# Kernel optimization log

Hardware: AMD Instinct MI355X
Metric: run time of the kernel (lower is better)

The kernel has to match this reference:

```python
import jax, jax.numpy as jnp
import numpy as np

B = 16
C = 80
LEVELS = [(128, 128, 8), (64, 64, 16), (32, 32, 32), (16, 16, 64), (8, 8, 128)]
TOPN = 1000
MIN_SCORE = 0.05
NMS_THR = 0.6
MAX_OBJ = 100


def setup_inputs() -> dict:
    key = jax.random.key(0)
    inp = {}
    for l, (H, W, s) in enumerate(LEVELS):
        key, k1, k2, k3 = jax.random.split(key, 4)
        inp[f"cls{l}"] = jax.random.uniform(k1, (B, H, W, C), jnp.float32)
        inp[f"reg{l}"] = jax.random.uniform(k2, (B, H, W, 4), jnp.float32) * 128.0
        inp[f"ctr{l}"] = jax.random.uniform(k3, (B, H, W, 1), jnp.float32)
        xs = (jnp.arange(W, dtype=jnp.float32) + 0.5) * s
        ys = (jnp.arange(H, dtype=jnp.float32) + 0.5) * s
        gx, gy = jnp.meshgrid(xs, ys)  # [H, W]
        pos = jnp.stack([gx, gy], axis=-1)  # [H, W, 2]
        inp[f"pos{l}"] = jnp.broadcast_to(pos, (B, H, W, 2))
    return inp


def _nms_one(scores, classes, bboxes):
    # scores [N], classes int32 [N], bboxes float [N, 4] (already int-truncated values)
    s = jnp.where(scores > MIN_SCORE, scores, -jnp.inf)  # score-threshold mask
    top_s, top_i = jax.lax.top_k(s, TOPN)  # sort descending, keep topn
    top_c = jax.lax.stop_gradient(classes[top_i].astype(jnp.float32))
    top_b = bboxes[top_i]
    valid = top_s > MIN_SCORE
    wh = top_b[:, 2:4] - top_b[:, 0:2]
    areas = jnp.clip(wh[:, 0] * wh[:, 1], 0.0001)
    ar = jnp.arange(TOPN)

    def body(i, suppressed):
        active = valid[i] & (~suppressed[i])
        b = top_b[i]
        tl = jnp.maximum(b[0:2], top_b[:, 0:2])
        br = jnp.minimum(b[2:4], top_b[:, 2:4])
        owh = jnp.clip(br - tl, 0.0)
        inter = owh[:, 0] * owh[:, 1]
        union = jnp.clip(areas[i] + areas - inter, 0.0001)
        iou = inter / union
        return suppressed | (active & (ar > i) & (iou >= NMS_THR))

    suppressed = jax.lax.fori_loop(0, TOPN, body, jnp.zeros((TOPN,), bool))
    keep = valid & (~suppressed)
    rank = jnp.cumsum(keep.astype(jnp.int32)) - 1
    # scatter kept detections (in score order) into first MAX_OBJ slots; slot MAX_OBJ is a dump
    idx = jnp.where(keep & (rank < MAX_OBJ), rank, MAX_OBJ)
    out_s = jnp.full((MAX_OBJ + 1,), -1.0, jnp.float32).at[idx].set(jnp.where(keep, top_s, -1.0))[:MAX_OBJ]
    out_c = jnp.full((MAX_OBJ + 1,), -1.0, jnp.float32).at[idx].set(jnp.where(keep, top_c, -1.0))[:MAX_OBJ]
    out_b = jnp.zeros((MAX_OBJ + 1, 4), jnp.float32).at[idx].set(jnp.where(keep[:, None], top_b, 0.0))[:MAX_OBJ]
    return out_s, out_c, out_b


def _forward(cls_list, reg_list, ctr_list, pos_list):
    ss, cc, bb = [], [], []
    for c, r, t, p in zip(cls_list, reg_list, ctr_list, pos_list):
        b = c.shape[0]
        c = c.reshape(b, -1, c.shape[-1])   # [B, HW, 80]
        r = r.reshape(b, -1, 4)             # [B, HW, 4]
        t = t.reshape(b, -1)                # [B, HW]
        p = p.reshape(b, -1, 2)             # [B, HW, 2]
        sc = jnp.sqrt(jnp.max(c, axis=2) * t)
        cl = jnp.argmax(c, axis=2).astype(jnp.int32)
        bmin = p - r[:, :, 0:2]
        bmax = p + r[:, :, 2:4]
        # torch .int() truncates toward zero; values are used as floats afterward
        box = jax.lax.stop_gradient(jnp.trunc(jnp.concatenate([bmin, bmax], axis=2)))
        ss.append(sc); cc.append(cl); bb.append(box)
    scores = jnp.concatenate(ss, axis=1)
    classes = jnp.concatenate(cc, axis=1)
    boxes = jnp.concatenate(bb, axis=1)
    return jax.vmap(_nms_one)(scores, classes, boxes)


def reference(cls0, cls1, cls2, cls3, cls4, reg0, reg1, reg2, reg3, reg4,
              ctr0, ctr1, ctr2, ctr3, ctr4, pos0, pos1, pos2, pos3, pos4):
    return _forward([cls0, cls1, cls2, cls3, cls4],
                    [reg0, reg1, reg2, reg3, reg4],
                    [ctr0, ctr1, ctr2, ctr3, ctr4],
                    [pos0, pos1, pos2, pos3, pos4])
```

## Files before the change

kernel.cpp:

```cpp
#include <hip/hip_runtime.h>
#include <stdint.h>

typedef unsigned int u32;
typedef unsigned long long u64;

#define NTOT 21824
#define NBATCH 16
#define TOPN 1000
#define MAXOBJ 100
#define CAPC 8192
#define NBINS 32768

__global__ __launch_bounds__(1024) void zero_kernel(u32* __restrict__ h) {
    int i = blockIdx.x * 1024 + threadIdx.x;
    if (i < NBATCH * NBINS + NBATCH * 32) h[i] = 0;
}

__global__ __launch_bounds__(256) void decode_kernel(
    const float* __restrict__ cls0, const float* __restrict__ cls1,
    const float* __restrict__ cls2, const float* __restrict__ cls3,
    const float* __restrict__ cls4,
    const float* __restrict__ ctr0, const float* __restrict__ ctr1,
    const float* __restrict__ ctr2, const float* __restrict__ ctr3,
    const float* __restrict__ ctr4,
    u32* __restrict__ keys, int* __restrict__ clsidx, u32* __restrict__ hist)
{
    int tid = threadIdx.x;
    int g = tid >> 2, j = tid & 3;
    int loc = blockIdx.x * 64 + g;
    int b = blockIdx.y;
    if (loc >= NTOT) return;

    const float *cp, *tp;
    if (loc < 16384)      { size_t o = (size_t)b*16384 + loc;          cp = cls0 + o*80; tp = ctr0 + o; }
    else if (loc < 20480) { size_t o = (size_t)b*4096  + (loc-16384);  cp = cls1 + o*80; tp = ctr1 + o; }
    else if (loc < 21504) { size_t o = (size_t)b*1024  + (loc-20480);  cp = cls2 + o*80; tp = ctr2 + o; }
    else if (loc < 21760) { size_t o = (size_t)b*256   + (loc-21504);  cp = cls3 + o*80; tp = ctr3 + o; }
    else                  { size_t o = (size_t)b*64    + (loc-21760);  cp = cls4 + o*80; tp = ctr4 + o; }

    const float4* c4 = (const float4*)cp;
    float maxv = -1.0f; int arg = 0;
#pragma unroll
    for (int q = 0; q < 5; ++q) {
        float4 v = c4[j + 4*q];
        int ch = 16*q + 4*j;
        if (v.x > maxv) { maxv = v.x; arg = ch;     }
        if (v.y > maxv) { maxv = v.y; arg = ch + 1; }
        if (v.z > maxv) { maxv = v.z; arg = ch + 2; }
        if (v.w > maxv) { maxv = v.w; arg = ch + 3; }
    }
#pragma unroll
    for (int d = 1; d <= 2; d <<= 1) {
        float ov = __shfl_xor(maxv, d);
        int   oa = __shfl_xor(arg, d);
        if (ov > maxv || (ov == maxv && oa < arg)) { maxv = ov; arg = oa; }
    }
    if (j == 0) {
        float score = sqrtf(maxv * (*tp));
        u32 key = (score > 0.05f) ? (__float_as_uint(score) | 0x80000000u) : 0u;
        size_t o = (size_t)b * NTOT + loc;
        keys[o] = key;
        clsidx[o] = arg;
        if (key) atomicAdd(&hist[b * NBINS + ((key >> 16) & (NBINS - 1))], 1u);
    }
}

__global__ __launch_bounds__(1024) void pivot_kernel(
    const u32* __restrict__ hist, u32* __restrict__ params,
    float* __restrict__ tscore, float* __restrict__ tcls, float4* __restrict__ tbox)
{
    __shared__ u32 s_wtot[16];
    __shared__ int s_tf;
    int b = blockIdx.x, tid = threadIdx.x;
    int lane = tid & 63, wave = tid >> 6;
    const u32* hb = hist + (size_t)b * NBINS;
    int base = tid * 32;

    for (int i = tid; i < TOPN; i += 1024) {
        size_t o = (size_t)b * TOPN + i;
        tscore[o] = -1.0f; tcls[o] = -1.0f;
        tbox[o] = make_float4(0.f, 0.f, 0.f, 0.f);
    }
    if (tid == 0) s_tf = -1;

    u32 s = 0;
#pragma unroll 8
    for (int j = 0; j < 32; ++j) s += hb[base + j];

    u32 x = s;
#pragma unroll
    for (int off = 1; off < 64; off <<= 1) {
        u32 y = __shfl_down(x, off);
        if (lane + off < 64) x += y;
    }
    if (lane == 0) s_wtot[wave] = x;
    __syncthreads();
    u32 wsuf = 0, tot = 0;
    for (int w2 = 0; w2 < 16; ++w2) { u32 v = s_wtot[w2]; tot += v; if (w2 > wave) wsuf += v; }
    u32 suffix_incl = x + wsuf;
    u32 suffix_above = suffix_incl - s;
    u32 target = (tot < TOPN) ? tot : TOPN;

    if (target > 0 && suffix_incl >= target) {
        u32 run = suffix_above;
        for (int j = 31; j >= 0; --j) {
            run += hb[base + j];
            if (run >= target) { atomicMax(&s_tf, base + j); break; }
        }
    }
    __syncthreads();
    if (tid == 0) {
        int t0 = s_tf;
        u32 P;
        if (target == 0)        P = 0xFFFFFFFFu;
        else if (tot <= TOPN)   P = 1u;
        else                    P = ((u32)t0 << 16) | 0x80000000u;
        params[2 * b] = P;
        params[2 * b + 1] = target;
    }
}

__global__ __launch_bounds__(256) void gather_kernel(
    const u32* __restrict__ keys, const u32* __restrict__ params,
    u64* __restrict__ candbuf, u32* __restrict__ gcnt)
{
    __shared__ u32 s_wcnt[4];
    __shared__ u32 s_base;
    int b = blockIdx.y;
    int tid = threadIdx.x;
    int lane = tid & 63, wave = tid >> 6;
    u32 P = params[2 * b];
    int i = blockIdx.x * 256 + tid;
    u32 k = (i < NTOT) ? keys[(size_t)b * NTOT + i] : 0u;
    bool pass = (k != 0u) && (k >= P);
    u64 mask = __ballot(pass);
    if (lane == 0) s_wcnt[wave] = (u32)__popcll(mask);
    __syncthreads();
    if (tid == 0) {
        u32 tot = s_wcnt[0] + s_wcnt[1] + s_wcnt[2] + s_wcnt[3];
        s_base = tot ? atomicAdd(&gcnt[b * 32], tot) : 0u;
    }
    __syncthreads();
    if (pass) {
        u32 woff = 0;
        for (int w2 = 0; w2 < wave; ++w2) woff += s_wcnt[w2];
        u32 pos = s_base + woff + (u32)__popcll(mask & ((1ull << lane) - 1ull));
        if (pos < CAPC)
            candbuf[(size_t)b * CAPC + pos] = ((u64)k << 32) | (u32)(~i);
    }
}

__global__ __launch_bounds__(256) void rank_kernel(
    const u64* __restrict__ candbuf, const u32* __restrict__ gcnt,
    const u32* __restrict__ params,
    const int* __restrict__ clsidx,
    const float* __restrict__ reg0, const float* __restrict__ reg1,
    const float* __restrict__ reg2, const float* __restrict__ reg3,
    const float* __restrict__ reg4,
    float* __restrict__ tscore, float* __restrict__ tcls, float4* __restrict__ tbox)
{
    int b = blockIdx.y;
    int lane = threadIdx.x & 63;
    u32 M = gcnt[b * 32]; if (M > CAPC) M = CAPC;
    u32 target = params[2 * b + 1];
    const u64* cb = candbuf + (size_t)b * CAPC;
    u32 Mr = (M + 63u) & ~63u;

    u32 wbase0 = blockIdx.x * 256 + (threadIdx.x & ~63u);
    for (u32 base = wbase0; base < M; base += 8 * 256) {
        u32 i0 = base + lane;
        bool val = (i0 < M);
        u64 e = val ? cb[i0] : ~0ull;
        u32 r = 0;
        for (u32 c0 = 0; c0 < Mr; c0 += 64) {
            u32 j = c0 + lane;
            u64 v = (j < M) ? cb[j] : 0ull;
            u32 vlo = (u32)v, vhi = (u32)(v >> 32);
#pragma unroll
            for (int s = 0; s < 64; ++s) {
                u32 lo = (u32)__builtin_amdgcn_readlane((int)vlo, s);
                u32 hi = (u32)__builtin_amdgcn_readlane((int)vhi, s);
                u64 vj = ((u64)hi << 32) | lo;
                r += (vj > e) ? 1u : 0u;
            }
        }
        if (val && r < target) {
            u32 k = (u32)(e >> 32);
            u32 loc = ~(u32)e;
            const float* rp; float st; u32 li; int wsh;
            if (loc < 16384u)      { li = loc;          wsh = 7; st = 8.f;   rp = reg0 + ((size_t)b*16384 + li)*4; }
            else if (loc < 20480u) { li = loc - 16384u; wsh = 6; st = 16.f;  rp = reg1 + ((size_t)b*4096  + li)*4; }
            else if (loc < 21504u) { li = loc - 20480u; wsh = 5; st = 32.f;  rp = reg2 + ((size_t)b*1024  + li)*4; }
            else if (loc < 21760u) { li = loc - 21504u; wsh = 4; st = 64.f;  rp = reg3 + ((size_t)b*256   + li)*4; }
            else                   { li = loc - 21760u; wsh = 3; st = 128.f; rp = reg4 + ((size_t)b*64    + li)*4; }
            u32 wx = li & ((1u << wsh) - 1u);
            u32 hy = li >> wsh;
            float px = ((float)wx + 0.5f) * st;
            float py = ((float)hy + 0.5f) * st;
            float4 rg = *(const float4*)rp;
            float4 bx;
            bx.x = truncf(px - rg.x); bx.y = truncf(py - rg.y);
            bx.z = truncf(px + rg.z); bx.w = truncf(py + rg.w);
            size_t src = (size_t)b * NTOT + loc;
            size_t o = (size_t)b * TOPN + r;
            tscore[o] = __uint_as_float(k & 0x7FFFFFFFu);
            tcls[o] = (float)clsidx[src];
            tbox[o] = bx;
        }
    }
}

__global__ __launch_bounds__(256) void iou_kernel(
    const float4* __restrict__ tbox, u64* __restrict__ sup)
{
    __shared__ float4 sbox[TOPN];
    int b = blockIdx.y;
    int tid = threadIdx.x, lane = tid & 63, wave = tid >> 6;
    const float4* tb = tbox + (size_t)b * TOPN;
    for (int i = tid; i < TOPN; i += 256) sbox[i] = tb[i];
    __syncthreads();
    int i = blockIdx.x * 4 + wave;
    float4 bi = sbox[i];
    float areai = fmaxf((bi.z - bi.x) * (bi.w - bi.y), 0.0001f);
    u64* row = sup + ((size_t)b * TOPN + i) * 16;
#pragma unroll
    for (int w = 0; w < 16; ++w) {
        int col = w * 64 + lane;
        bool bit = false;
        if (col < TOPN) {
            float4 bj = sbox[col];
            float areaj = fmaxf((bj.z - bj.x) * (bj.w - bj.y), 0.0001f);
            float tlx = fmaxf(bi.x, bj.x), tly = fmaxf(bi.y, bj.y);
            float brx = fminf(bi.z, bj.z), bry = fminf(bi.w, bj.w);
            float ow = fmaxf(brx - tlx, 0.f), oh = fmaxf(bry - tly, 0.f);
            float inter = ow * oh;
            float uni = fmaxf(areai + areaj - inter, 0.0001f);
            bit = (col > i) && (inter / uni >= 0.6f);
        }
        u64 m = __ballot(bit);
        if (lane == 0) row[w] = m;
    }
}

#define CHROWS 128
#define NCHUNK 8

__global__ __launch_bounds__(1024) void finalize_kernel(
    const float* __restrict__ tscore, const float* __restrict__ tcls,
    const float4* __restrict__ tbox, const u64* __restrict__ sup,
    float* __restrict__ out)
{
    __shared__ u64 mat[2][CHROWS * 16];
    __shared__ u32 validsh[TOPN];
    __shared__ u64 removed_sh[16];
    __shared__ u32 wpref[17];
    int b = blockIdx.x, tid = threadIdx.x;
    int wave = tid >> 6, lane = tid & 63;

    for (int i = tid; i < TOPN; i += 1024)
        validsh[i] = (tscore[(size_t)b * TOPN + i] > 0.05f) ? 1u : 0u;

    const u64* supb = sup + (size_t)b * TOPN * 16;
    for (int idx = tid; idx < CHROWS * 16; idx += 1024)
        mat[0][idx] = supb[idx];
    __syncthreads();

    u64 my = 0;
    if (wave == 0) {
#pragma unroll
        for (int w2 = 0; w2 < 16; ++w2) {
            int i = w2 * 64 + lane;
            bool v = (i < TOPN) ? (validsh[i] != 0) : false;
            u64 m = __ballot(v);
            if (lane == w2) my = ~m;
        }
    }

    for (int chunk = 0; chunk < NCHUNK; ++chunk) {
        if (wave > 0 && chunk + 1 < NCHUNK) {
            int nr = (chunk + 1 == NCHUNK - 1) ? (TOPN - (NCHUNK - 1) * CHROWS) : CHROWS;
            const u64* src = supb + (size_t)(chunk + 1) * CHROWS * 16;
            u64* dst = mat[(chunk + 1) & 1];
            for (int idx = tid - 64; idx < nr * 16; idx += 960)
                dst[idx] = src[idx];
        }
        if (wave == 0) {
            int r0 = chunk * CHROWS;
            int rows = (chunk == NCHUNK - 1) ? (TOPN - r0) : CHROWS;
            int lw = lane & 15;
            const u64* M = mat[chunk & 1];
            for (int sub = 0; sub < rows; sub += 64) {
                int w2 = (r0 + sub) >> 6;
                u64 cur = __shfl(my, w2);
                int nsub = rows - sub; if (nsub > 64) nsub = 64;
                const u64* R = M + sub * 16;
                int ngrp = nsub >> 3;
                u64 cme[8], cww[8];
#pragma unroll
                for (int g = 0; g < 8; ++g) { cme[g] = R[g*16 + lw]; cww[g] = R[g*16 + w2]; }
                for (int grp = 0; grp < ngrp; ++grp) {
                    u64 nme[8] = {0,0,0,0,0,0,0,0}, nww[8] = {0,0,0,0,0,0,0,0};
                    if (grp + 1 < ngrp) {
                        const u64* Rn = R + (grp + 1) * 128;
#pragma unroll
                        for (int g = 0; g < 8; ++g) { nme[g] = Rn[g*16 + lw]; nww[g] = Rn[g*16 + w2]; }
                    }
#pragma unroll
                    for (int g = 0; g < 8; ++g) {
                        int u = grp * 8 + g;
                        u64 bit = (cur >> u) & 1ull;
                        u64 act = bit - 1ull;
                        cur |= cww[g] & act;
                        my  |= cme[g] & act;
                    }
#pragma unroll
                    for (int g = 0; g < 8; ++g) { cme[g] = nme[g]; cww[g] = nww[g]; }
                }
            }
        }
        __syncthreads();
    }
    if (wave == 0) {
        if (lane < 16) removed_sh[lane] = my;
        u32 pc = (lane < 16) ? (u32)__popcll(~my) : 0u;
#pragma unroll
        for (int off = 1; off < 16; off <<= 1) {
            u32 y = __shfl_up(pc, off);
            if (lane >= off) pc += y;
        }
        if (lane < 16) wpref[lane + 1] = pc;
        if (lane == 0) wpref[0] = 0;
    }
    __syncthreads();

    float* out_s = out;
    float* out_c = out + NBATCH * MAXOBJ;
    float* out_b = out + 2 * NBATCH * MAXOBJ;
    if (tid < MAXOBJ)     { out_s[b * MAXOBJ + tid] = -1.f; out_c[b * MAXOBJ + tid] = -1.f; }
    if (tid < MAXOBJ * 4) out_b[b * MAXOBJ * 4 + tid] = 0.f;
    __syncthreads();
    if (tid < TOPN) {
        u64 kw = ~removed_sh[tid >> 6];
        if ((kw >> (tid & 63)) & 1ull) {
            int rank = (int)wpref[tid >> 6] + (int)__popcll(kw & ((1ull << (tid & 63)) - 1ull));
            if (rank < MAXOBJ) {
                size_t o = (size_t)b * TOPN + tid;
                out_s[b * MAXOBJ + rank] = tscore[o];
                out_c[b * MAXOBJ + rank] = tcls[o];
                ((float4*)out_b)[b * MAXOBJ + rank] = tbox[o];
            }
        }
    }
}

extern "C" void kernel_launch(void* const* d_in, const int* in_sizes, int n_in,
                              void* d_out, int out_size, void* d_ws, size_t ws_size,
                              hipStream_t stream) {
    (void)in_sizes; (void)n_in; (void)out_size; (void)ws_size;
    const float* cls[5]; const float* reg[5]; const float* ctr[5];
    for (int l = 0; l < 5; ++l) {
        cls[l] = (const float*)d_in[4 * l + 0];
        reg[l] = (const float*)d_in[4 * l + 1];
        ctr[l] = (const float*)d_in[4 * l + 2];
    }
    char* w = (char*)d_ws;
    u32*    keys   = (u32*)(w + 0);
    int*    clsidx = (int*)(w + 1396736);
    float*  tscore = (float*)(w + 2793472);
    float*  tcls   = (float*)(w + 2857472);
    float4* tbox   = (float4*)(w + 2921472);
    u64*    sup    = (u64*)(w + 3177472);
    u64*    candbuf= (u64*)(w + 3177472);
    u32*    hist   = (u32*)(w + 5225472);
    u32*    gcnt   = (u32*)(w + 7322624);
    u32*    params = (u32*)(w + 7324672);

    zero_kernel<<<(NBATCH * NBINS + NBATCH * 32 + 1023) / 1024, 1024, 0, stream>>>(hist);
    decode_kernel<<<dim3((NTOT + 63) / 64, NBATCH), 256, 0, stream>>>(
        cls[0], cls[1], cls[2], cls[3], cls[4],
        ctr[0], ctr[1], ctr[2], ctr[3], ctr[4],
        keys, clsidx, hist);
    pivot_kernel<<<NBATCH, 1024, 0, stream>>>(hist, params, tscore, tcls, tbox);
    gather_kernel<<<dim3((NTOT + 255) / 256, NBATCH), 256, 0, stream>>>(keys, params, candbuf, gcnt);
    rank_kernel<<<dim3(8, NBATCH), 256, 0, stream>>>(candbuf, gcnt, params, clsidx,
                                                     reg[0], reg[1], reg[2], reg[3], reg[4],
                                                     tscore, tcls, tbox);
    iou_kernel<<<dim3(TOPN / 4, NBATCH), 256, 0, stream>>>(tbox, sup);
    finalize_kernel<<<NBATCH, 1024, 0, stream>>>(tscore, tcls, tbox, sup, (float*)d_out);
}
```

Before: 295.9 us.

## Move score histogram into pivot kernel shared memory and drop zero kernel

Removes the global 32768-bin histogram and its zeroing kernel. The pivot kernel now reads the keys and builds a 1024-bin histogram in shared memory over a clamped exponent range starting at BINBASE. The decode kernel has no atomics and processes two locations per thread group so more loads are in flight. The cost is that each pivot block scans all keys for its batch serially, and clamping to the lowest bin assumes scores sit within the binned range, which the score threshold and sqrt keep true.

```diff
diff --git a/kernel.cpp b/kernel.cpp
--- a/kernel.cpp
+++ b/kernel.cpp
@@ -9,11 +9,24 @@
 #define TOPN 1000
 #define MAXOBJ 100
 #define CAPC 8192
-#define NBINS 32768
-
-__global__ __launch_bounds__(1024) void zero_kernel(u32* __restrict__ h) {
-    int i = blockIdx.x * 1024 + threadIdx.x;
-    if (i < NBATCH * NBINS + NBATCH * 32) h[i] = 0;
+#define BINBASE 15616
+#define NBINS 1024
+
+__device__ __forceinline__ void locate(
+    int b, int loc,
+    const float* __restrict__ cls0, const float* __restrict__ cls1,
+    const float* __restrict__ cls2, const float* __restrict__ cls3,
+    const float* __restrict__ cls4,
+    const float* __restrict__ ctr0, const float* __restrict__ ctr1,
+    const float* __restrict__ ctr2, const float* __restrict__ ctr3,
+    const float* __restrict__ ctr4,
+    const float*& cp, const float*& tp)
+{
+    if (loc < 16384)      { size_t o = (size_t)b*16384 + loc;          cp = cls0 + o*80; tp = ctr0 + o; }
+    else if (loc < 20480) { size_t o = (size_t)b*4096  + (loc-16384);  cp = cls1 + o*80; tp = ctr1 + o; }
+    else if (loc < 21504) { size_t o = (size_t)b*1024  + (loc-20480);  cp = cls2 + o*80; tp = ctr2 + o; }
+    else if (loc < 21760) { size_t o = (size_t)b*256   + (loc-21504);  cp = cls3 + o*80; tp = ctr3 + o; }
+    else                  { size_t o = (size_t)b*64    + (loc-21760);  cp = cls4 + o*80; tp = ctr4 + o; }
 }
 
 __global__ __launch_bounds__(256) void decode_kernel(
@@ -23,71 +36,106 @@
     const float* __restrict__ ctr0, const float* __restrict__ ctr1,
     const float* __restrict__ ctr2, const float* __restrict__ ctr3,
     const float* __restrict__ ctr4,
-    u32* __restrict__ keys, int* __restrict__ clsidx, u32* __restrict__ hist)
+    u32* __restrict__ keys, int* __restrict__ clsidx)
 {
     int tid = threadIdx.x;
     int g = tid >> 2, j = tid & 3;
-    int loc = blockIdx.x * 64 + g;
     int b = blockIdx.y;
-    if (loc >= NTOT) return;
-
-    const float *cp, *tp;
-    if (loc < 16384)      { size_t o = (size_t)b*16384 + loc;          cp = cls0 + o*80; tp = ctr0 + o; }
-    else if (loc < 20480) { size_t o = (size_t)b*4096  + (loc-16384);  cp = cls1 + o*80; tp = ctr1 + o; }
-    else if (loc < 21504) { size_t o = (size_t)b*1024  + (loc-20480);  cp = cls2 + o*80; tp = ctr2 + o; }
-    else if (loc < 21760) { size_t o = (size_t)b*256   + (loc-21504);  cp = cls3 + o*80; tp = ctr3 + o; }
-    else                  { size_t o = (size_t)b*64    + (loc-21760);  cp = cls4 + o*80; tp = ctr4 + o; }
-
-    const float4* c4 = (const float4*)cp;
-    float maxv = -1.0f; int arg = 0;
+    int loc0 = blockIdx.x * 128 + g;
+    int loc1 = loc0 + 64;
+    bool v1 = (loc1 < NTOT);
+
+    const float *cp0, *tp0, *cp1, *tp1;
+    locate(b, loc0, cls0, cls1, cls2, cls3, cls4, ctr0, ctr1, ctr2, ctr3, ctr4, cp0, tp0);
+    locate(b, v1 ? loc1 : loc0, cls0, cls1, cls2, cls3, cls4, ctr0, ctr1, ctr2, ctr3, ctr4, cp1, tp1);
+
+    const float4* c40 = (const float4*)cp0;
+    const float4* c41 = (const float4*)cp1;
+    float4 a0[5], a1[5];
+#pragma unroll
+    for (int q = 0; q < 5; ++q) a0[q] = c40[j + 4*q];
+#pragma unroll
+    for (int q = 0; q < 5; ++q) a1[q] = c41[j + 4*q];
+    float t0v = *tp0;
+    float t1v = *tp1;
+
+    float maxv0 = -1.0f; int arg0 = 0;
+    float maxv1 = -1.0f; int arg1 = 0;
 #pragma unroll
     for (int q = 0; q < 5; ++q) {
-        float4 v = c4[j + 4*q];
+        float4 v = a0[q];
         int ch = 16*q + 4*j;
-        if (v.x > maxv) { maxv = v.x; arg = ch;     }
-        if (v.y > maxv) { maxv = v.y; arg = ch + 1; }
-        if (v.z > maxv) { maxv = v.z; arg = ch + 2; }
-        if (v.w > maxv) { maxv = v.w; arg = ch + 3; }
+        if (v.x > maxv0) { maxv0 = v.x; arg0 = ch;     }
+        if (v.y > maxv0) { maxv0 = v.y; arg0 = ch + 1; }
+        if (v.z > maxv0) { maxv0 = v.z; arg0 = ch + 2; }
+        if (v.w > maxv0) { maxv0 = v.w; arg0 = ch + 3; }
+    }
+#pragma unroll
+    for (int q = 0; q < 5; ++q) {
+        float4 v = a1[q];
+        int ch = 16*q + 4*j;
+        if (v.x > maxv1) { maxv1 = v.x; arg1 = ch;     }
+        if (v.y > maxv1) { maxv1 = v.y; arg1 = ch + 1; }
+        if (v.z > maxv1) { maxv1 = v.z; arg1 = ch + 2; }
+        if (v.w > maxv1) { maxv1 = v.w; arg1 = ch + 3; }
     }
 #pragma unroll
     for (int d = 1; d <= 2; d <<= 1) {
-        float ov = __shfl_xor(maxv, d);
-        int   oa = __shfl_xor(arg, d);
-        if (ov > maxv || (ov == maxv && oa < arg)) { maxv = ov; arg = oa; }
+        float ov = __shfl_xor(maxv0, d);
+        int   oa = __shfl_xor(arg0, d);
+        if (ov > maxv0 || (ov == maxv0 && oa < arg0)) { maxv0 = ov; arg0 = oa; }
+        float ow = __shfl_xor(maxv1, d);
+        int   ob = __shfl_xor(arg1, d);
+        if (ow > maxv1 || (ow == maxv1 && ob < arg1)) { maxv1 = ow; arg1 = ob; }
     }
     if (j == 0) {
-        float score = sqrtf(maxv * (*tp));
-        u32 key = (score > 0.05f) ? (__float_as_uint(score) | 0x80000000u) : 0u;
-        size_t o = (size_t)b * NTOT + loc;
-        keys[o] = key;
-        clsidx[o] = arg;
-        if (key) atomicAdd(&hist[b * NBINS + ((key >> 16) & (NBINS - 1))], 1u);
+        float score0 = sqrtf(maxv0 * t0v);
+        u32 key0 = (score0 > 0.05f) ? (__float_as_uint(score0) | 0x80000000u) : 0u;
+        size_t o0 = (size_t)b * NTOT + loc0;
+        keys[o0] = key0;
+        clsidx[o0] = arg0;
+        if (v1) {
+            float score1 = sqrtf(maxv1 * t1v);
+            u32 key1 = (score1 > 0.05f) ? (__float_as_uint(score1) | 0x80000000u) : 0u;
+            size_t o1 = (size_t)b * NTOT + loc1;
+            keys[o1] = key1;
+            clsidx[o1] = arg1;
+        }
     }
 }
 
 __global__ __launch_bounds__(1024) void pivot_kernel(
-    const u32* __restrict__ hist, u32* __restrict__ params,
+    const u32* __restrict__ keys, u32* __restrict__ params, u32* __restrict__ gcnt,
     float* __restrict__ tscore, float* __restrict__ tcls, float4* __restrict__ tbox)
 {
+    __shared__ u32 shist[NBINS];
     __shared__ u32 s_wtot[16];
     __shared__ int s_tf;
     int b = blockIdx.x, tid = threadIdx.x;
     int lane = tid & 63, wave = tid >> 6;
-    const u32* hb = hist + (size_t)b * NBINS;
-    int base = tid * 32;
+    const u32* kb = keys + (size_t)b * NTOT;
 
     for (int i = tid; i < TOPN; i += 1024) {
         size_t o = (size_t)b * TOPN + i;
         tscore[o] = -1.0f; tcls[o] = -1.0f;
         tbox[o] = make_float4(0.f, 0.f, 0.f, 0.f);
     }
-    if (tid == 0) s_tf = -1;
-
-    u32 s = 0;
-#pragma unroll 8
-    for (int j = 0; j < 32; ++j) s += hb[base + j];
-
-    u32 x = s;
+    shist[tid] = 0;
+    if (tid == 0) { s_tf = -1; gcnt[b * 32] = 0; }
+    __syncthreads();
+
+    for (int i = tid; i < NTOT; i += 1024) {
+        u32 k = kb[i];
+        if (k) {
+            int v = (int)((k >> 16) & 0x7FFFu) - BINBASE;
+            v = v < 0 ? 0 : (v > NBINS - 1 ? NBINS - 1 : v);
+            atomicAdd(&shist[v], 1u);
+        }
+    }
+    __syncthreads();
+
+    u32 h = shist[tid];
+    u32 x = h;
 #pragma unroll
     for (int off = 1; off < 64; off <<= 1) {
         u32 y = __shfl_down(x, off);
@@ -98,23 +146,16 @@
     u32 wsuf = 0, tot = 0;
     for (int w2 = 0; w2 < 16; ++w2) { u32 v = s_wtot[w2]; tot += v; if (w2 > wave) wsuf += v; }
     u32 suffix_incl = x + wsuf;
-    u32 suffix_above = suffix_incl - s;
     u32 target = (tot < TOPN) ? tot : TOPN;
 
-    if (target > 0 && suffix_incl >= target) {
-        u32 run = suffix_above;
-        for (int j = 31; j >= 0; --j) {
-            run += hb[base + j];
-            if (run >= target) { atomicMax(&s_tf, base + j); break; }
-        }
-    }
+    if (target > 0 && suffix_incl >= target) atomicMax(&s_tf, tid);
     __syncthreads();
     if (tid == 0) {
         int t0 = s_tf;
         u32 P;
         if (target == 0)        P = 0xFFFFFFFFu;
         else if (tot <= TOPN)   P = 1u;
-        else                    P = ((u32)t0 << 16) | 0x80000000u;
+        else                    P = ((u32)(t0 + BINBASE) << 16) | 0x80000000u;
         params[2 * b] = P;
         params[2 * b + 1] = target;
     }
@@ -371,16 +412,14 @@
     float4* tbox   = (float4*)(w + 2921472);
     u64*    sup    = (u64*)(w + 3177472);
     u64*    candbuf= (u64*)(w + 3177472);
-    u32*    hist   = (u32*)(w + 5225472);
-    u32*    gcnt   = (u32*)(w + 7322624);
-    u32*    params = (u32*)(w + 7324672);
-
-    zero_kernel<<<(NBATCH * NBINS + NBATCH * 32 + 1023) / 1024, 1024, 0, stream>>>(hist);
-    decode_kernel<<<dim3((NTOT + 63) / 64, NBATCH), 256, 0, stream>>>(
+    u32*    gcnt   = (u32*)(w + 5225472);
+    u32*    params = (u32*)(w + 5227520);
+
+    decode_kernel<<<dim3((NTOT + 127) / 128, NBATCH), 256, 0, stream>>>(
         cls[0], cls[1], cls[2], cls[3], cls[4],
         ctr[0], ctr[1], ctr[2], ctr[3], ctr[4],
-        keys, clsidx, hist);
-    pivot_kernel<<<NBATCH, 1024, 0, stream>>>(hist, params, tscore, tcls, tbox);
+        keys, clsidx);
+    pivot_kernel<<<NBATCH, 1024, 0, stream>>>(keys, params, gcnt, tscore, tcls, tbox);
     gather_kernel<<<dim3((NTOT + 255) / 256, NBATCH), 256, 0, stream>>>(keys, params, candbuf, gcnt);
     rank_kernel<<<dim3(8, NBATCH), 256, 0, stream>>>(candbuf, gcnt, params, clsidx,
                                                      reg[0], reg[1], reg[2], reg[3], reg[4],
```

Measured after the change: 269.6 us. -8.9%, faster.
